# Kernel tuning notes

Hardware: AMD Instinct MI355X
Metric: run time of the kernel (lower is better)

Reference implementation:

```python
import jax, jax.numpy as jnp
import numpy as np
from jax import lax


def ternary_quantize(w):
    # alpha = mean(|w|); threshold = 0.7*alpha; map to {-1,0,1}*alpha
    alpha = jnp.mean(jnp.abs(w))
    threshold = 0.7 * alpha
    w_ternary = jnp.where(jnp.abs(w) < threshold, jnp.zeros_like(w), jnp.sign(w))
    return alpha * w_ternary


def setup_inputs() -> dict:
    key = jax.random.key(0)
    k1, k2 = jax.random.split(key)
    B, L, Cin = 32, 8192, 1
    K, F = 16, 256
    x = jax.random.normal(k1, (B, L, Cin), dtype=jnp.float32)
    # matches keras RandomUniform(-0.1, 0.1) initializer
    w = jax.random.uniform(k2, (K, Cin, F), dtype=jnp.float32, minval=-0.1, maxval=0.1)
    b = jnp.zeros((F,), dtype=jnp.float32)
    return {"x": x, "w": w, "b": b}


def reference(x, w, b):
    # x: (B, L, Cin) NWC; w: (K, Cin, F) WIO; stride 1, padding SAME
    w_q = ternary_quantize(w)
    y = lax.conv_general_dilated(
        x, w_q,
        window_strides=(1,),
        padding="SAME",
        dimension_numbers=("NWC", "WIO", "NWC"),
    )
    return y + b
```

## Files before the change

### kernel.cpp

```cpp
#include <hip/hip_runtime.h>
#include <hip/hip_bf16.h>

typedef float f32x4 __attribute__((ext_vector_type(4)));

__global__ __launch_bounds__(256) void ternary_conv1d_fused(
    const float* __restrict__ x,
    const float* __restrict__ w,
    const float* __restrict__ bias,
    float* __restrict__ y,
    int L) {
    const int t  = threadIdx.x;
    const int fg = t & 63;
    const int ls = t >> 6;
    const int bid = blockIdx.x;
    const int b  = bid >> 6;
    const int g  = bid & 63;
    const int lbase = g * 128;

    __shared__ float xs[144];

    if (t < 143) {
        int gl = lbase - 7 + t;
        xs[t] = (gl >= 0 && gl < L) ? x[(size_t)b * L + gl] : 0.f;
    }

    f32x4 wv[16];
    float s = 0.f;
#pragma unroll
    for (int k = 0; k < 16; ++k) {
        f32x4 v = *reinterpret_cast<const f32x4*>(w + k * 256 + fg * 4);
        wv[k] = v;
        s += fabsf(v.x) + fabsf(v.y) + fabsf(v.z) + fabsf(v.w);
    }
#pragma unroll
    for (int m = 1; m < 64; m <<= 1) s += __shfl_xor(s, m, 64);
    const float alpha = s * (1.0f / 4096.0f);
    const float thr = 0.7f * alpha;

#pragma unroll
    for (int k = 0; k < 16; ++k) {
        f32x4 v = wv[k], q;
#pragma unroll
        for (int c = 0; c < 4; ++c) {
            float vc = v[c];
            q[c] = (fabsf(vc) < thr) ? 0.f
                 : (vc > 0.f ? alpha : (vc < 0.f ? -alpha : 0.f));
        }
        wv[k] = q;
    }
    const f32x4 bv = *reinterpret_cast<const f32x4*>(bias + fg * 4);

    __syncthreads();

    float xw[16];
#pragma unroll
    for (int j = 0; j < 16; ++j) xw[j] = xs[ls + j];

    f32x4* outp = reinterpret_cast<f32x4*>(y) + ((size_t)b * L + lbase + ls) * 64 + fg;
#pragma unroll
    for (int i = 0; i < 32; ++i) {
        f32x4 acc = bv;
#pragma unroll
        for (int k = 0; k < 16; ++k) {
            acc += wv[k] * xw[k];
        }
        *outp = acc;
        outp += 256;
        if (i < 31) {
#pragma unroll
            for (int j = 0; j < 12; ++j) xw[j] = xw[j + 4];
#pragma unroll
            for (int j = 12; j < 16; ++j) xw[j] = xs[ls + 4 * (i + 1) + j];
        }
    }
}

extern "C" void kernel_launch(void* const* d_in, const int* in_sizes, int n_in,
                              void* d_out, int out_size, void* d_ws, size_t ws_size,
                              hipStream_t stream) {
    const float* x = (const float*)d_in[0];
    const float* w = (const float*)d_in[1];
    const float* b = (const float*)d_in[2];
    float* y = (float*)d_out;

    const int B = 32;
    const int L = in_sizes[0] / B;

    ternary_conv1d_fused<<<B * 64, 256, 0, stream>>>(x, w, b, y, L);
}
```

Before: 52.03 us.

## Split waves into producer/consumer roles with double-buffered LDS staging for output

Result: faster. 50.20 us (-3.5%).

```diff
diff --git a/kernel.cpp b/kernel.cpp
--- a/kernel.cpp
+++ b/kernel.cpp
@@ -3,75 +3,101 @@
 
 typedef float f32x4 __attribute__((ext_vector_type(4)));
 
-__global__ __launch_bounds__(256) void ternary_conv1d_fused(
+__global__ __launch_bounds__(512, 2) void ternary_conv1d_pc(
     const float* __restrict__ x,
     const float* __restrict__ w,
     const float* __restrict__ bias,
     float* __restrict__ y,
     int L) {
-    const int t  = threadIdx.x;
-    const int fg = t & 63;
-    const int ls = t >> 6;
-    const int bid = blockIdx.x;
-    const int b  = bid >> 6;
-    const int g  = bid & 63;
-    const int lbase = g * 128;
+    const int t    = threadIdx.x;
+    const int lane = t & 63;
+    const int wid  = t >> 6;
+    const int bid  = blockIdx.x;
+    const int b    = bid >> 4;
+    const int g    = bid & 15;
+    const int lbase = g * 512;
 
-    __shared__ float xs[144];
+    __shared__ float xs[528];
+    __shared__ float buf[2][32][256];
 
-    if (t < 143) {
-        int gl = lbase - 7 + t;
-        xs[t] = (gl >= 0 && gl < L) ? x[(size_t)b * L + gl] : 0.f;
+    const size_t xb = (size_t)b * L;
+    for (int j = t; j < 527; j += 512) {
+        int gl = lbase - 7 + j;
+        xs[j] = (gl >= 0 && gl < L) ? x[xb + gl] : 0.f;
     }
 
-    f32x4 wv[16];
-    float s = 0.f;
+    f32x4 wq[16];
+    f32x4 bv;
+    if (wid < 4) {
+        float s = 0.f;
 #pragma unroll
-    for (int k = 0; k < 16; ++k) {
-        f32x4 v = *reinterpret_cast<const f32x4*>(w + k * 256 + fg * 4);
-        wv[k] = v;
-        s += fabsf(v.x) + fabsf(v.y) + fabsf(v.z) + fabsf(v.w);
+        for (int k = 0; k < 16; ++k) {
+            f32x4 v = *reinterpret_cast<const f32x4*>(w + k * 256 + lane * 4);
+            wq[k] = v;
+            s += fabsf(v.x) + fabsf(v.y) + fabsf(v.z) + fabsf(v.w);
+        }
+#pragma unroll
+        for (int m = 1; m < 64; m <<= 1) s += __shfl_xor(s, m, 64);
+        const float alpha = s * (1.0f / 4096.0f);
+        const float thr = 0.7f * alpha;
+#pragma unroll
+        for (int k = 0; k < 16; ++k) {
+            f32x4 v = wq[k], q;
+#pragma unroll
+            for (int c = 0; c < 4; ++c) {
+                float vc = v[c];
+                q[c] = (fabsf(vc) < thr) ? 0.f
+                     : (vc > 0.f ? alpha : (vc < 0.f ? -alpha : 0.f));
+            }
+            wq[k] = q;
+        }
+        bv = *reinterpret_cast<const f32x4*>(bias + lane * 4);
     }
-#pragma unroll
-    for (int m = 1; m < 64; m <<= 1) s += __shfl_xor(s, m, 64);
-    const float alpha = s * (1.0f / 4096.0f);
-    const float thr = 0.7f * alpha;
-
-#pragma unroll
-    for (int k = 0; k < 16; ++k) {
-        f32x4 v = wv[k], q;
-#pragma unroll
-        for (int c = 0; c < 4; ++c) {
-            float vc = v[c];
-            q[c] = (fabsf(vc) < thr) ? 0.f
-                 : (vc > 0.f ? alpha : (vc < 0.f ? -alpha : 0.f));
-        }
-        wv[k] = q;
-    }
-    const f32x4 bv = *reinterpret_cast<const f32x4*>(bias + fg * 4);
 
     __syncthreads();
 
-    float xw[16];
+    auto produce = [&](int c) {
+        const int cb = c & 1;
+        const int r0 = wid * 8;
+        const int base = c * 32 + r0;
+        float xw[16];
 #pragma unroll
-    for (int j = 0; j < 16; ++j) xw[j] = xs[ls + j];
+        for (int j = 0; j < 16; ++j) xw[j] = xs[base + j];
+#pragma unroll
+        for (int i = 0; i < 8; ++i) {
+            f32x4 acc = bv;
+#pragma unroll
+            for (int k = 0; k < 16; ++k) acc += wq[k] * xw[k];
+            *reinterpret_cast<f32x4*>(&buf[cb][r0 + i][lane * 4]) = acc;
+            if (i < 7) {
+#pragma unroll
+                for (int j = 0; j < 15; ++j) xw[j] = xw[j + 1];
+                xw[15] = xs[base + i + 16];
+            }
+        }
+    };
 
-    f32x4* outp = reinterpret_cast<f32x4*>(y) + ((size_t)b * L + lbase + ls) * 64 + fg;
+    auto consume = [&](int c) {
+        const int cb = c & 1;
+        const int r0 = (wid - 4) * 8;
+        float* out0 = y + ((size_t)b * L + lbase + c * 32 + r0) * 256 + lane * 4;
 #pragma unroll
-    for (int i = 0; i < 32; ++i) {
-        f32x4 acc = bv;
-#pragma unroll
-        for (int k = 0; k < 16; ++k) {
-            acc += wv[k] * xw[k];
+        for (int i = 0; i < 8; ++i) {
+            f32x4 v = *reinterpret_cast<const f32x4*>(&buf[cb][r0 + i][lane * 4]);
+            *reinterpret_cast<f32x4*>(out0 + (size_t)i * 256) = v;
         }
-        *outp = acc;
-        outp += 256;
-        if (i < 31) {
-#pragma unroll
-            for (int j = 0; j < 12; ++j) xw[j] = xw[j + 4];
-#pragma unroll
-            for (int j = 12; j < 16; ++j) xw[j] = xs[ls + 4 * (i + 1) + j];
+    };
+
+    if (wid < 4) produce(0);
+    __syncthreads();
+
+    for (int c = 0; c < 16; ++c) {
+        if (wid < 4) {
+            if (c < 15) produce(c + 1);
+        } else {
+            consume(c);
         }
+        __syncthreads();
     }
 }
 
@@ -86,5 +112,5 @@
     const int B = 32;
     const int L = in_sizes[0] / B;
 
-    ternary_conv1d_fused<<<B * 64, 256, 0, stream>>>(x, w, b, y, L);
+    ternary_conv1d_pc<<<B * 16, 512, 0, stream>>>(x, w, b, y, L);
 }
```
